# Kernel optimization log

Measured on AMD Instinct MI355X. Metric: run time of the kernel, lower is better.

## Reference

```python
import jax, jax.numpy as jnp
import numpy as np

CAUSAL = True


def setup_inputs() -> dict:
    key = jax.random.key(0)
    k1, k2, k3 = jax.random.split(key, 3)
    B, S, D_IN, D_INNER, D_OUT = 4, 4096, 512, 64, 512
    x = jax.random.normal(k1, (B, S, D_IN), dtype=jnp.float32)
    W_qkv = jax.random.normal(k2, (D_IN, 3 * D_INNER), dtype=jnp.float32) * (D_IN ** -0.5)
    W_out = jax.random.normal(k3, (D_INNER, D_OUT), dtype=jnp.float32) * (D_INNER ** -0.5)
    b_out = jnp.zeros((D_OUT,), dtype=jnp.float32)
    return {"x": x, "W_qkv": W_qkv, "W_out": W_out, "b_out": b_out}


def reference(x, W_qkv, W_out, b_out):
    d_inner = W_out.shape[0]
    scale = d_inner ** -0.5
    qkv = jnp.einsum('bsi,io->bso', x, W_qkv)  # [B,S,3*d_inner]
    q, k, v = jnp.split(qkv, 3, axis=-1)
    sim = jnp.einsum('bid,bjd->bij', q, k) * scale  # [B,S,S]
    if CAUSAL:
        S = x.shape[1]
        mask = jnp.triu(jnp.ones((S, S), dtype=bool), k=1)
        sim = jnp.where(mask[None], -jnp.finfo(q.dtype).max, sim)
    attn = jax.nn.softmax(sim, axis=-1)
    out = jnp.einsum('bij,bjd->bid', attn, v)  # [B,S,d_inner]
    return jnp.einsum('bid,do->bio', out, W_out) + b_out
```

## Files before the change

### kernel.cpp

```cpp
#include <hip/hip_runtime.h>
#include <math.h>

typedef __attribute__((ext_vector_type(8))) short short8;
typedef __attribute__((ext_vector_type(4))) short short4v;
typedef __attribute__((ext_vector_type(4))) float f32x4;
typedef __attribute__((ext_vector_type(4))) float float4v;

__device__ __forceinline__ unsigned short f2bf(float f){
  unsigned int u = __float_as_uint(f);
  u += 0x7FFFu + ((u >> 16) & 1u);
  return (unsigned short)(u >> 16);
}
__device__ __forceinline__ float bf2f(short s){
  return __uint_as_float(((unsigned int)(unsigned short)s) << 16);
}

typedef __attribute__((address_space(1))) const unsigned char* gas_t;
typedef __attribute__((address_space(3))) unsigned char* las_t;
__device__ __forceinline__ void async16(const void* g, void* l) {
  __builtin_amdgcn_global_load_lds((gas_t)g, (las_t)l, 16, 0, 0);
}

#define SC2 0.1803368801111204f

__global__ __launch_bounds__(256) void prep_w(
    const float* __restrict__ Wqkv, const float* __restrict__ Wout,
    unsigned short* __restrict__ Wtq, unsigned short* __restrict__ Wto)
{
  int idx = blockIdx.x * 256 + threadIdx.x;
  if (idx < 192 * 512) {
    int n = idx >> 9, k = idx & 511;
    Wtq[idx] = f2bf(Wqkv[k * 192 + n]);
  } else {
    int i2 = idx - 192 * 512;
    int n = i2 >> 6, k = i2 & 63;
    Wto[i2] = f2bf(Wout[k * 512 + n]);
  }
}

__global__ __launch_bounds__(256) void qkv_kernel(
    const float* __restrict__ x,
    const unsigned short* __restrict__ Wt,
    unsigned short* __restrict__ qg,
    unsigned short* __restrict__ kg,
    unsigned short* __restrict__ vT)
{
  __shared__ __align__(16) unsigned short Wb[64][128];
  __shared__ __align__(16) unsigned short vbuf[64][72];
  const int part = blockIdx.x % 3;
  const int rb   = blockIdx.x / 3;
  const int lane = threadIdx.x & 63;
  const int wave = threadIdx.x >> 6;
  const int mrow = lane & 15;
  const int quad = lane >> 4;
  const int mb = rb * 64;
  const int m0 = mb + wave * 16;
  const int sw = mrow & 7;

  const int srow = lane >> 4;
  const int sch  = lane & 15;
#define STAGE_W(s)                                                            \
  {                                                                           \
    _Pragma("unroll")                                                         \
    for (int ii = 0; ii < 4; ii++) {                                          \
      const int r0 = wave * 16 + ii * 4;                                      \
      const int r  = r0 + srow;                                               \
      const int cd = (sch & 8) | ((sch ^ (r & 7)) & 7);                       \
      async16(Wt + (size_t)(part * 64 + r) * 512 + (s) * 128 + cd * 8,        \
              &Wb[r0][0]);                                                    \
    }                                                                         \
  }

  STAGE_W(0)

  f32x4 acc[4];
#pragma unroll
  for (int t = 0; t < 4; t++) acc[t] = (f32x4){0.f, 0.f, 0.f, 0.f};
  const float* xp = x + (size_t)(m0 + mrow) * 512 + quad * 8;

  for (int s = 0; s < 4; s++) {
    __syncthreads();
#pragma unroll
    for (int l = 0; l < 4; l++) {
      const int kk = s * 4 + l;
      float4v a0 = *(const float4v*)(xp + kk * 32);
      float4v a1 = *(const float4v*)(xp + kk * 32 + 4);
      short8 af;
#pragma unroll
      for (int j = 0; j < 4; j++) { af[j] = (short)f2bf(a0[j]); af[4 + j] = (short)f2bf(a1[j]); }
      const int c   = l * 4 + quad;
      const int pos = (c & 8) | ((c ^ sw) & 7);
#pragma unroll
      for (int t = 0; t < 4; t++) {
        short8 bf = *(const short8*)(&Wb[t * 16 + mrow][0] + pos * 8);
        acc[t] = __builtin_amdgcn_mfma_f32_16x16x32_bf16(af, bf, acc[t], 0, 0, 0);
      }
    }
    __syncthreads();
    if (s < 3) STAGE_W(s + 1)
  }

#pragma unroll
  for (int t = 0; t < 4; t++)
#pragma unroll
    for (int r = 0; r < 4; r++)
      vbuf[wave * 16 + quad * 4 + r][t * 16 + mrow] = f2bf(acc[t][r]);
  __syncthreads();

  if (part < 2) {
    unsigned short* dst = part ? kg : qg;
    const int row = threadIdx.x >> 2;
    const int seg = (threadIdx.x & 3) * 16;
    short8 w0 = *(const short8*)&vbuf[row][seg];
    short8 w1 = *(const short8*)&vbuf[row][seg + 8];
    unsigned short* p = dst + (size_t)(mb + row) * 64 + seg;
    *(short8*)(p) = w0;
    *(short8*)(p + 8) = w1;
  } else {
    const int d  = threadIdx.x >> 2;
    const int s8 = (threadIdx.x & 3) * 16;
    const int bb = rb >> 6;
    const int sb = mb & 4095;
    short8 w0, w1;
#pragma unroll
    for (int i = 0; i < 8; i++) {
      w0[i] = (short)vbuf[s8 + i][d];
      w1[i] = (short)vbuf[s8 + 8 + i][d];
    }
    unsigned short* dst = vT + (size_t)bb * (64 * 4096) + (size_t)d * 4096 + sb + s8;
    *(short8*)(dst) = w0;
    *(short8*)(dst + 8) = w1;
  }
#undef STAGE_W
}

template <bool MASKED>
__device__ __forceinline__ void soft_pv(
    const f32x4* sA, const short8* vf, int kb, int qlane, int quad, int mrow,
    float& lacc, f32x4* o, unsigned short (*pb)[72])
{
  float p[16];
#pragma unroll
  for (int t = 0; t < 4; t++)
#pragma unroll
    for (int r = 0; r < 4; r++) {
      float v = sA[t][r];
      if (MASKED && (kb + t * 16 + quad * 4 + r > qlane)) v = -3.0e38f;
      p[t * 4 + r] = exp2f(v * SC2);
    }
  float ps = 0.f;
#pragma unroll
  for (int i = 0; i < 16; i++) ps += p[i];
  lacc += ps;
#pragma unroll
  for (int t = 0; t < 4; t++) {
    short4v pk;
#pragma unroll
    for (int r = 0; r < 4; r++) pk[r] = (short)f2bf(p[t * 4 + r]);
    *(short4v*)&pb[mrow][t * 16 + quad * 4] = pk;
  }
  short8 pf0 = *(const short8*)&pb[mrow][quad * 8];
  short8 pf1 = *(const short8*)&pb[mrow][32 + quad * 8];
#pragma unroll
  for (int c = 0; c < 4; c++) {
    o[c] = __builtin_amdgcn_mfma_f32_16x16x32_bf16(vf[2 * c],     pf0, o[c], 0, 0, 0);
    o[c] = __builtin_amdgcn_mfma_f32_16x16x32_bf16(vf[2 * c + 1], pf1, o[c], 0, 0, 0);
  }
}

__global__ __launch_bounds__(256) void attn_kernel(
    const unsigned short* __restrict__ qg,
    const unsigned short* __restrict__ kg,
    const unsigned short* __restrict__ vT,
    unsigned short* __restrict__ Opart,
    float* __restrict__ lpart)
{
  __shared__ __align__(16) unsigned short Kb[2][64][64];
  __shared__ __align__(16) unsigned short Vb[2][64][64];
  __shared__ __align__(16) unsigned short pbuf[4][16][72];
  const int lane = threadIdx.x & 63;
  const int wave = threadIdx.x >> 6;
  const int mrow = lane & 15;
  const int quad = lane >> 4;
  const int sw   = mrow & 7;

  int t = 143 - (blockIdx.x % 144);
  const int b = blockIdx.x / 144;
  int qj = 31, c = 0;
  for (int qq = 0; qq < 32; qq++) {
    const int ncq = (qq >> 2) + 1;
    if (t < ncq) { qj = qq; c = t; break; }
    t -= ncq;
  }

  const int sq0w = qj * 128 + wave * 32;
  const int g0w  = b * 4096 + sq0w;

  short8 qf[2][2];
#pragma unroll
  for (int s = 0; s < 2; s++) {
    const unsigned short* qp = qg + (size_t)(g0w + 16 * s + mrow) * 64 + quad * 8;
    qf[s][0] = *(const short8*)(qp);
    qf[s][1] = *(const short8*)(qp + 32);
  }

  const int kstart = c << 9;
  const int qend   = qj * 128 + 128;
  const int kend   = (kstart + 512 < qend) ? (kstart + 512) : qend;
  const int nTb    = (kend - kstart) >> 6;

  f32x4 o[2][4];
#pragma unroll
  for (int s = 0; s < 2; s++)
#pragma unroll
    for (int ct = 0; ct < 4; ct++) o[s][ct] = (f32x4){0.f, 0.f, 0.f, 0.f};
  float lr[2] = {0.f, 0.f};

  const unsigned short* kbase = kg + (size_t)b * 4096 * 64;
  const unsigned short* vbase = vT + (size_t)b * 64 * 4096;
  const int shalf = lane >> 3;
  const int sch   = lane & 7;

#define STAGE_KV(kb, Kd, Vd)                                                  \
  {                                                                           \
    _Pragma("unroll")                                                         \
    for (int ii = 0; ii < 2; ii++) {                                          \
      const int r0 = wave * 16 + ii * 8;                                      \
      const int r  = r0 + shalf;                                              \
      const int cd = sch ^ (r & 7);                                           \
      async16(kbase + (size_t)((kb) + r) * 64 + cd * 8, (Kd) + r0 * 64);      \
      async16(vbase + (size_t)r * 4096 + (kb) + cd * 8, (Vd) + r0 * 64);      \
    }                                                                         \
  }

  STAGE_KV(kstart, &Kb[0][0][0], &Vb[0][0][0])
  __syncthreads();

  for (int j = 0; j < nTb; j++) {
    const int kb = kstart + 64 * j;
    if (j + 1 < nTb)
      STAGE_KV(kb + 64, &Kb[(j + 1) & 1][0][0], &Vb[(j + 1) & 1][0][0])
    const unsigned short* Kc = &Kb[j & 1][0][0];
    const unsigned short* Vc = &Vb[j & 1][0][0];

    short8 kf[8];
#pragma unroll
    for (int tt = 0; tt < 4; tt++) {
      const unsigned short* kr = Kc + (tt * 16 + mrow) * 64;
      kf[2 * tt]     = *(const short8*)(kr + (quad ^ sw) * 8);
      kf[2 * tt + 1] = *(const short8*)(kr + ((quad + 4) ^ sw) * 8);
    }
    f32x4 sA[2][4];
    bool act[2];
#pragma unroll
    for (int s = 0; s < 2; s++) {
      act[s] = (kb <= sq0w + 16 * s + 15);
      if (act[s]) {
#pragma unroll
        for (int tt = 0; tt < 4; tt++) {
          f32x4 z = (f32x4){0.f, 0.f, 0.f, 0.f};
          z = __builtin_amdgcn_mfma_f32_16x16x32_bf16(kf[2 * tt],     qf[s][0], z, 0, 0, 0);
          z = __builtin_amdgcn_mfma_f32_16x16x32_bf16(kf[2 * tt + 1], qf[s][1], z, 0, 0, 0);
          sA[s][tt] = z;
        }
      }
    }
    short8 vf[8];
#pragma unroll
    for (int cc = 0; cc < 4; cc++) {
      const unsigned short* vr = Vc + (cc * 16 + mrow) * 64;
      vf[2 * cc]     = *(const short8*)(vr + (quad ^ sw) * 8);
      vf[2 * cc + 1] = *(const short8*)(vr + ((quad + 4) ^ sw) * 8);
    }
#pragma unroll
    for (int s = 0; s < 2; s++) {
      if (!act[s]) continue;
      const int qlo = sq0w + 16 * s;
      if (kb + 63 <= qlo)
        soft_pv<false>(sA[s], vf, kb, qlo + mrow, quad, mrow, lr[s], o[s], pbuf[wave]);
      else
        soft_pv<true> (sA[s], vf, kb, qlo + mrow, quad, mrow, lr[s], o[s], pbuf[wave]);
    }
    __syncthreads();
  }
#undef STAGE_KV

#pragma unroll
  for (int s = 0; s < 2; s++) {
    float lt = lr[s];
    lt += __shfl_xor(lt, 16);
    lt += __shfl_xor(lt, 32);
    const size_t row = (size_t)c * 16384 + g0w + 16 * s + mrow;
#pragma unroll
    for (int ct = 0; ct < 4; ct++) {
      short4v ob;
#pragma unroll
      for (int r = 0; r < 4; r++) ob[r] = (short)f2bf(o[s][ct][r]);
      *(short4v*)(Opart + row * 64 + ct * 16 + quad * 4) = ob;
    }
    if (quad == 0) lpart[row] = lt;
  }
}

__global__ __launch_bounds__(256) void combine_kernel(
    const unsigned short* __restrict__ Opart,
    const float* __restrict__ lpart,
    const unsigned short* __restrict__ WtO,
    const float* __restrict__ bias,
    float* __restrict__ out)
{
  __shared__ __align__(16) unsigned short Wob[128][64];
  __shared__ __align__(16) float obuf[4][16][132];
  const int lane = threadIdx.x & 63;
  const int wave = threadIdx.x >> 6;
  const int mrow = lane & 15;
  const int quad = lane >> 4;
  const int rb = blockIdx.x >> 2;
  const int ch = blockIdx.x & 3;
  const int g0 = rb * 64 + wave * 16;
  const int nc = ((g0 & 4095) >> 9) + 1;

  {
    const int half = lane >> 3;
    const int chp  = lane & 7;
#pragma unroll
    for (int ii = 0; ii < 4; ii++) {
      const int r0 = wave * 32 + ii * 8;
      const int r  = r0 + half;
      const int cd = chp ^ (r & 7);
      async16(WtO + (size_t)(ch * 128 + r) * 64 + cd * 8, &Wob[r0][0]);
    }
  }

  float L = 0.f;
  f32x4 A0 = (f32x4){0,0,0,0}, A1 = A0, A2 = A0, A3 = A0;
  for (int cI = 0; cI < nc; cI++) {
    const size_t row = (size_t)cI * 16384 + g0 + mrow;
    L += lpart[row];
    const unsigned short* op = Opart + row * 64 + quad * 8;
    short8 x0 = *(const short8*)(op);
    short8 x1 = *(const short8*)(op + 32);
#pragma unroll
    for (int j = 0; j < 4; j++) {
      A0[j] += bf2f(x0[j]); A1[j] += bf2f(x0[4 + j]);
      A2[j] += bf2f(x1[j]); A3[j] += bf2f(x1[4 + j]);
    }
  }
  const float inv = 1.0f / L;
  short8 of0, of1;
#pragma unroll
  for (int i = 0; i < 4; i++) {
    of0[i]     = (short)f2bf(A0[i] * inv);
    of0[i + 4] = (short)f2bf(A1[i] * inv);
    of1[i]     = (short)f2bf(A2[i] * inv);
    of1[i + 4] = (short)f2bf(A3[i] * inv);
  }
  __syncthreads();

  const int sw = mrow & 7;
#pragma unroll
  for (int t = 0; t < 8; t++) {
    const int n = ch * 128 + t * 16 + mrow;
    const unsigned short* wr = &Wob[t * 16 + mrow][0];
    short8 w0 = *(const short8*)(wr + (quad ^ sw) * 8);
    short8 w1 = *(const short8*)(wr + ((quad + 4) ^ sw) * 8);
    f32x4 pr = (f32x4){0,0,0,0};
    pr = __builtin_amdgcn_mfma_f32_16x16x32_bf16(of0, w0, pr, 0, 0, 0);
    pr = __builtin_amdgcn_mfma_f32_16x16x32_bf16(of1, w1, pr, 0, 0, 0);
    const float bv = bias[n];
#pragma unroll
    for (int r = 0; r < 4; r++)
      obuf[wave][quad * 4 + r][t * 16 + mrow] = pr[r] + bv;
  }
#pragma unroll
  for (int j = 0; j < 4; j++) {
#pragma unroll
    for (int h = 0; h < 2; h++) {
      const int row = 4 * j + (lane >> 4);
      const int col = 4 * (lane & 15) + 64 * h;
      float4v v = *(const float4v*)&obuf[wave][row][col];
      *(float4v*)(out + (size_t)(g0 + row) * 512 + ch * 128 + col) = v;
    }
  }
}

extern "C" void kernel_launch(void* const* d_in, const int* in_sizes, int n_in,
                              void* d_out, int out_size, void* d_ws, size_t ws_size,
                              hipStream_t stream) {
  const float* x    = (const float*)d_in[0];
  const float* Wqkv = (const float*)d_in[1];
  const float* Wout = (const float*)d_in[2];
  const float* bout = (const float*)d_in[3];
  float* out = (float*)d_out;

  unsigned short* q   = (unsigned short*)d_ws;
  unsigned short* k   = q   + 16384 * 64;
  unsigned short* vT  = k   + 16384 * 64;
  unsigned short* Wtq = vT  + 4 * 64 * 4096;
  unsigned short* Wto = Wtq + 192 * 512;
  unsigned short* Opart = Wto + 512 * 64;
  float* lprt = (float*)(Opart + (size_t)8 * 16384 * 64);

  prep_w<<<512, 256, 0, stream>>>(Wqkv, Wout, Wtq, Wto);
  qkv_kernel<<<768, 256, 0, stream>>>(x, Wtq, q, k, vT);
  attn_kernel<<<576, 256, 0, stream>>>(q, k, vT, Opart, lprt);
  combine_kernel<<<1024, 256, 0, stream>>>(Opart, lprt, Wto, bout, out);
}
```

Before: 149.4 us.

## Compute all of Q, K, V per block to read x once, with double-buffered weights

The QKV projection kernel now has each block compute all three 64-column outputs (q, k, v) for its 64 rows instead of splitting them across three blocks. This removes the threefold re-read and bf16 conversion of x. The weight tile is double-buffered in LDS with 64-wide k-chunks, so the prefetch of the next chunk overlaps the MFMAs on the current one. In exchange the grid shrinks from 768 to 256 blocks, and the 12 accumulators raise register pressure, which may lower occupancy and parallelism on a large GPU.

```diff
diff --git a/kernel.cpp b/kernel.cpp
--- a/kernel.cpp
+++ b/kernel.cpp
@@ -45,10 +45,9 @@
     unsigned short* __restrict__ kg,
     unsigned short* __restrict__ vT)
 {
-  __shared__ __align__(16) unsigned short Wb[64][128];
+  __shared__ __align__(16) unsigned short Wb[2][192][64];
   __shared__ __align__(16) unsigned short vbuf[64][72];
-  const int part = blockIdx.x % 3;
-  const int rb   = blockIdx.x / 3;
+  const int rb   = blockIdx.x;
   const int lane = threadIdx.x & 63;
   const int wave = threadIdx.x >> 6;
   const int mrow = lane & 15;
@@ -57,79 +56,82 @@
   const int m0 = mb + wave * 16;
   const int sw = mrow & 7;
 
-  const int srow = lane >> 4;
-  const int sch  = lane & 15;
-#define STAGE_W(s)                                                            \
+  const int srow = lane >> 3;
+  const int sch  = lane & 7;
+#define STAGE_W(s, dst)                                                       \
   {                                                                           \
     _Pragma("unroll")                                                         \
-    for (int ii = 0; ii < 4; ii++) {                                          \
-      const int r0 = wave * 16 + ii * 4;                                      \
+    for (int ii = 0; ii < 6; ii++) {                                          \
+      const int r0 = wave * 48 + ii * 8;                                      \
       const int r  = r0 + srow;                                               \
-      const int cd = (sch & 8) | ((sch ^ (r & 7)) & 7);                       \
-      async16(Wt + (size_t)(part * 64 + r) * 512 + (s) * 128 + cd * 8,        \
-              &Wb[r0][0]);                                                    \
+      const int cd = sch ^ (r & 7);                                           \
+      async16(Wt + (size_t)r * 512 + (s) * 64 + cd * 8, (dst) + r0 * 64);     \
     }                                                                         \
   }
 
-  STAGE_W(0)
-
-  f32x4 acc[4];
-#pragma unroll
-  for (int t = 0; t < 4; t++) acc[t] = (f32x4){0.f, 0.f, 0.f, 0.f};
+  STAGE_W(0, &Wb[0][0][0])
+
+  f32x4 acc[12];
+#pragma unroll
+  for (int t = 0; t < 12; t++) acc[t] = (f32x4){0.f, 0.f, 0.f, 0.f};
   const float* xp = x + (size_t)(m0 + mrow) * 512 + quad * 8;
 
-  for (int s = 0; s < 4; s++) {
+  for (int s = 0; s < 8; s++) {
     __syncthreads();
-#pragma unroll
-    for (int l = 0; l < 4; l++) {
-      const int kk = s * 4 + l;
+    if (s < 7) STAGE_W(s + 1, &Wb[(s + 1) & 1][0][0])
+    const unsigned short* Wc = &Wb[s & 1][0][0];
+#pragma unroll
+    for (int l = 0; l < 2; l++) {
+      const int kk = s * 2 + l;
       float4v a0 = *(const float4v*)(xp + kk * 32);
       float4v a1 = *(const float4v*)(xp + kk * 32 + 4);
       short8 af;
 #pragma unroll
       for (int j = 0; j < 4; j++) { af[j] = (short)f2bf(a0[j]); af[4 + j] = (short)f2bf(a1[j]); }
       const int c   = l * 4 + quad;
-      const int pos = (c & 8) | ((c ^ sw) & 7);
-#pragma unroll
-      for (int t = 0; t < 4; t++) {
-        short8 bf = *(const short8*)(&Wb[t * 16 + mrow][0] + pos * 8);
+      const int pos = (c ^ sw) & 7;
+#pragma unroll
+      for (int t = 0; t < 12; t++) {
+        short8 bf = *(const short8*)(Wc + (t * 16 + mrow) * 64 + pos * 8);
         acc[t] = __builtin_amdgcn_mfma_f32_16x16x32_bf16(af, bf, acc[t], 0, 0, 0);
       }
     }
+  }
+
+#pragma unroll
+  for (int p = 0; p < 3; p++) {
     __syncthreads();
-    if (s < 3) STAGE_W(s + 1)
-  }
-
-#pragma unroll
-  for (int t = 0; t < 4; t++)
-#pragma unroll
-    for (int r = 0; r < 4; r++)
-      vbuf[wave * 16 + quad * 4 + r][t * 16 + mrow] = f2bf(acc[t][r]);
-  __syncthreads();
-
-  if (part < 2) {
-    unsigned short* dst = part ? kg : qg;
-    const int row = threadIdx.x >> 2;
-    const int seg = (threadIdx.x & 3) * 16;
-    short8 w0 = *(const short8*)&vbuf[row][seg];
-    short8 w1 = *(const short8*)&vbuf[row][seg + 8];
-    unsigned short* p = dst + (size_t)(mb + row) * 64 + seg;
-    *(short8*)(p) = w0;
-    *(short8*)(p + 8) = w1;
-  } else {
-    const int d  = threadIdx.x >> 2;
-    const int s8 = (threadIdx.x & 3) * 16;
-    const int bb = rb >> 6;
-    const int sb = mb & 4095;
-    short8 w0, w1;
-#pragma unroll
-    for (int i = 0; i < 8; i++) {
-      w0[i] = (short)vbuf[s8 + i][d];
-      w1[i] = (short)vbuf[s8 + 8 + i][d];
-    }
-    unsigned short* dst = vT + (size_t)bb * (64 * 4096) + (size_t)d * 4096 + sb + s8;
-    *(short8*)(dst) = w0;
-    *(short8*)(dst + 8) = w1;
+#pragma unroll
+    for (int t4 = 0; t4 < 4; t4++)
+#pragma unroll
+      for (int r = 0; r < 4; r++)
+        vbuf[wave * 16 + quad * 4 + r][t4 * 16 + mrow] = f2bf(acc[p * 4 + t4][r]);
+    __syncthreads();
+
+    if (p < 2) {
+      unsigned short* dst = p ? kg : qg;
+      const int row = threadIdx.x >> 2;
+      const int seg = (threadIdx.x & 3) * 16;
+      short8 w0 = *(const short8*)&vbuf[row][seg];
+      short8 w1 = *(const short8*)&vbuf[row][seg + 8];
+      unsigned short* pd = dst + (size_t)(mb + row) * 64 + seg;
+      *(short8*)(pd) = w0;
+      *(short8*)(pd + 8) = w1;
+    } else {
+      const int d  = threadIdx.x >> 2;
+      const int s8 = (threadIdx.x & 3) * 16;
+      const int bb = rb >> 6;
+      const int sb = mb & 4095;
+      short8 w0, w1;
+#pragma unroll
+      for (int i = 0; i < 8; i++) {
+        w0[i] = (short)vbuf[s8 + i][d];
+        w1[i] = (short)vbuf[s8 + 8 + i][d];
+      }
+      unsigned short* dst = vT + (size_t)bb * (64 * 4096) + (size_t)d * 4096 + sb + s8;
+      *(short8*)(dst) = w0;
+      *(short8*)(dst + 8) = w1;
+    }
   }
 #undef STAGE_W
 }
@@ -402,7 +404,7 @@
   float* lprt = (float*)(Opart + (size_t)8 * 16384 * 64);
 
   prep_w<<<512, 256, 0, stream>>>(Wqkv, Wout, Wtq, Wto);
-  qkv_kernel<<<768, 256, 0, stream>>>(x, Wtq, q, k, vT);
+  qkv_kernel<<<256, 256, 0, stream>>>(x, Wtq, q, k, vT);
   attn_kernel<<<576, 256, 0, stream>>>(q, k, vT, Opart, lprt);
   combine_kernel<<<1024, 256, 0, stream>>>(Opart, lprt, Wto, bout, out);
 }
```

New measurement: 152.3 us. About the same (+1.9%).
